# Kernel optimization log

Hardware: AMD Instinct MI355X
Metric: run time of the kernel (lower is better)

The kernel has to match this reference:

```python
import jax, jax.numpy as jnp
import numpy as np

K = 3        # prediction_steps
SKIP = 1     # skip_step (forward default)
NEG = 64     # opt.negative_samples
EPS = 1e-11  # ExpNLLLoss epsilon


def setup_inputs() -> dict:
    key = jax.random.key(0)
    ks = jax.random.split(key, 8)
    B, C, H, W = 64, 256, 14, 14
    z = jax.random.normal(ks[0], (B, C, H, W), jnp.float32)
    c = jax.random.normal(ks[1], (B, C, H, W), jnp.float32)
    Wk = jax.random.normal(ks[2], (K, C, C), jnp.float32) / np.sqrt(C).astype(np.float32)
    inp = {"z": z, "c": c, "Wk": Wk}
    for k in range(1, K + 1):
        Hp = H - (k + SKIP)
        rows = Hp * W * B
        inp[f"neg_idx_k{k}"] = jax.random.randint(ks[2 + k], (rows * NEG,), 0, rows, dtype=jnp.int32)
    return inp


def _loss_k(z, c, Wk, neg_idx, k):
    # z, c: [B,C,H,W]; Wk: [Co,Ci] (1x1 conv); neg_idx: [(H-k-SKIP)*W*B*NEG]
    B, C, H, W = z.shape
    Hp = H - (k + SKIP)
    zt = z[:, :, k + SKIP:, :]                            # [B,Ci,Hp,W]
    ztwk = jnp.einsum('oc,bchw->hwbo', Wk, zt)            # [Hp,W,B,Co] (1x1 conv + permute(2,3,0,1))
    flat = ztwk.reshape(Hp * W * B, -1)
    shuf = flat[neg_idx].reshape(Hp, W, B, NEG, -1)       # gathered negatives [Hp,W,B,N,Co]
    ctx = jnp.transpose(c[:, :, :Hp, :], (2, 3, 0, 1))    # context c[:,:,:-(k+SKIP),:] -> [Hp,W,B,Co]
    main = jnp.einsum('hwbc,hwbc->hwb', ctx, ztwk)[..., None]   # [Hp,W,B,1]
    negs = jnp.einsum('hwbc,hwbnc->hwbn', ctx, shuf)            # [Hp,W,B,N]
    log_fk = jnp.concatenate([main, negs], axis=-1)             # [Hp,W,B,1+N]
    log_fk = jnp.transpose(log_fk, (2, 3, 0, 1))                # [B,1+N,Hp,W]
    probs = jax.nn.softmax(log_fk, axis=1)
    # ExpNLLLoss, target class 0, reduction='mean'
    return -jnp.mean(jnp.log(probs[:, 0] + EPS))


def reference(z, c, Wk, neg_idx_k1, neg_idx_k2, neg_idx_k3):
    idxs = [neg_idx_k1, neg_idx_k2, neg_idx_k3]
    total = 0.0
    for k in range(1, K + 1):
        total = total + _loss_k(z, c, Wk[k - 1], idxs[k - 1], k)
    return total / K
```

## Files before the change

kernel.cpp:

```cpp
#include <hip/hip_runtime.h>
#include <math.h>


typedef short bf16x8 __attribute__((ext_vector_type(8)));
typedef float f32x4 __attribute__((ext_vector_type(4)));

static __device__ __forceinline__ unsigned short f2bf(float f) {
    union { float f; unsigned int u; } x; x.f = f;
    unsigned int r = x.u + 0x7fffu + ((x.u >> 16) & 1u);
    return (unsigned short)(r >> 16);
}

static __device__ __forceinline__ unsigned char f2e4m3(float f) {
    union { float f; unsigned int u; } x; x.f = f;
    unsigned int s = (x.u >> 24) & 0x80u;
    float af = fabsf(f);
    if (af > 448.f) af = 448.f;
    x.f = af;
    unsigned int u = x.u;
    int e = (int)(u >> 23) - 127;
    unsigned int out;
    if (af == 0.f) {
        out = 0u;
    } else if (e < -6) {
        int mq = (int)rintf(af * 512.f);
        out = (mq >= 8) ? 0x08u : (unsigned int)mq;
    } else {
        unsigned int r = u + 0x7FFFFu + ((u >> 20) & 1u);
        int e2 = (int)(r >> 23) - 127;
        if (e2 > 8) out = 0x7Eu;
        else out = (unsigned int)(((e2 + 7) << 3) | ((r >> 20) & 7u));
    }
    return (unsigned char)(s | out);
}

static __device__ __forceinline__ void gload_lds4(const void* g, void* l) {
    __builtin_amdgcn_global_load_lds(
        (const __attribute__((address_space(1))) void*)g,
        (__attribute__((address_space(3))) void*)l, 4, 0, 0);
}

__global__ __launch_bounds__(256)
void prep_kernel(const float* __restrict__ z, const float* __restrict__ c,
                 const float* __restrict__ Wk,
                 unsigned short* __restrict__ zt, unsigned char* __restrict__ ct8,
                 unsigned short* __restrict__ wkb, float* __restrict__ out) {
    __shared__ float tile[16][201];
    const int tid = threadIdx.x;
    int x = blockIdx.x;
    if (x < 768) {
        int i = x * 256 + tid;
        wkb[i] = f2bf(Wk[i]);
        if (x == 0 && tid == 0) out[0] = 0.f;
        return;
    }
    const bool isz = x < 1792;
    const int local = isz ? (x - 768) : (x - 1792);
    const float* src = isz ? z : c;
    const int b  = local & 63;
    const int c0 = (local >> 6) << 4;
    for (int i = tid; i < 16 * 196; i += 256) {
        int cc = i / 196;
        int hw = i - cc * 196;
        tile[cc][hw] = src[(size_t)((b << 8) + c0 + cc) * 196 + hw];
    }
    __syncthreads();
    if (isz) {
        for (int i = tid; i < 196 * 16; i += 256) {
            int hw = i >> 4, cc = i & 15;
            zt[(size_t)((hw << 6) + b) * 256 + c0 + cc] = f2bf(tile[cc][hw]);
        }
    } else {
        for (int i = tid; i < 196 * 16; i += 256) {
            int hw = i >> 4, cc = i & 15;
            ct8[(size_t)((hw << 6) + b) * 256 + c0 + cc] = f2e4m3(tile[cc][hw]);
        }
    }
}

#define PSTR 544
__global__ __launch_bounds__(256)
void proj_mfma_kernel(const unsigned short* __restrict__ zt,
                      const unsigned short* __restrict__ wkb,
                      unsigned char* __restrict__ ztwk) {
    __shared__ __align__(16) unsigned char smem[(64 + 32) * PSTR];
    unsigned char* smA = smem;
    unsigned char* smB = smem + 64 * PSTR;

    int x = blockIdx.x;
    int k, hw;
    if (x < 168)      { k = 0; hw = x; }
    else if (x < 322) { k = 1; hw = x - 168; }
    else              { k = 2; hw = x - 322; }
    const int o0 = blockIdx.y << 5;
    const int row0  = hw << 6;
    const int zrow0 = row0 + (((k + 2) * 14) << 6);
    unsigned char* zo = ztwk + (size_t)k * 10752 * 256;

    const int tid = threadIdx.x;
    const unsigned char* zsrc = (const unsigned char*)(zt + (size_t)zrow0 * 256);
    const unsigned char* bsrc = (const unsigned char*)(wkb + ((size_t)k << 16) + o0 * 256);

    #pragma unroll
    for (int i = 0; i < 8; ++i) {
        int sb = ((i << 8) + tid) << 4;
        int r = sb >> 9, off = sb & 511;
        *(int4*)(smA + r * PSTR + off) = *(const int4*)(zsrc + sb);
    }
    #pragma unroll
    for (int i = 0; i < 4; ++i) {
        int sb = ((i << 8) + tid) << 4;
        int r = sb >> 9, off = sb & 511;
        *(int4*)(smB + r * PSTR + off) = *(const int4*)(bsrc + sb);
    }
    __syncthreads();

    const int wv = tid >> 6, lane = tid & 63;
    const int m = lane & 15, kq = lane >> 4;
    f32x4 acc[2] = {};
    const unsigned short* aP  = (const unsigned short*)(smA + (size_t)((wv << 4) + m) * PSTR) + (kq << 3);
    const unsigned short* bP0 = (const unsigned short*)(smB + (size_t)m * PSTR) + (kq << 3);
    const unsigned short* bP1 = (const unsigned short*)(smB + (size_t)(16 + m) * PSTR) + (kq << 3);
    #pragma unroll
    for (int kk = 0; kk < 256; kk += 32) {
        bf16x8 af = *(const bf16x8*)(aP  + kk);
        bf16x8 b0 = *(const bf16x8*)(bP0 + kk);
        bf16x8 b1 = *(const bf16x8*)(bP1 + kk);
        acc[0] = __builtin_amdgcn_mfma_f32_16x16x32_bf16(af, b0, acc[0], 0, 0, 0);
        acc[1] = __builtin_amdgcn_mfma_f32_16x16x32_bf16(af, b1, acc[1], 0, 0, 0);
    }
    __syncthreads();
    unsigned char* cs = smA;
    #pragma unroll
    for (int nt = 0; nt < 2; ++nt)
        #pragma unroll
        for (int r = 0; r < 4; ++r)
            cs[(size_t)((wv << 4) + (kq << 2) + r) * 40 + (nt << 4) + m] =
                f2e4m3(acc[nt][r]);
    __syncthreads();
    {
        int r = tid >> 2, off = (tid & 3) << 3;
        unsigned long long v = *(const unsigned long long*)(cs + (size_t)r * 40 + off);
        *(unsigned long long*)(zo + (size_t)(row0 + r) * 256 + o0 + off) = v;
    }
}

#define ROWB 272
#define SLABSZ (65 * ROWB + 272)
__global__ __launch_bounds__(128)
void loss_mfma_kernel(const unsigned char* __restrict__ ct8,
                      const unsigned char* __restrict__ ztwk8,
                      const int* __restrict__ n0, const int* __restrict__ n1,
                      const int* __restrict__ n2, float* __restrict__ rowloss) {
    __shared__ __align__(16) unsigned char lds[2][SLABSZ];
    const int tid = threadIdx.x;
    const int wv = tid >> 6, lane = tid & 63;
    const int m = lane & 15, kq = lane >> 4;
    unsigned char* sl  = lds[wv];
    unsigned char* ctx = sl + 65 * ROWB;

    const int W = (blockIdx.x << 1) + wv;
    const int base = W << 3;
    int k; const int* nb; int segbase;
    if (base < 10752)      { k = 0; nb = n0; segbase = 0; }
    else if (base < 20608) { k = 1; nb = n1; segbase = 10752; }
    else                   { k = 2; nb = n2; segbase = 20608; }
    const int row0 = base - segbase;
    const unsigned char* flat8 = ztwk8 + (size_t)k * 10752 * 256;
    const float wkf = (k == 0) ? (1.f / (3.f * 10752.f))
                    : (k == 1) ? (1.f / (3.f * 9856.f))
                               : (1.f / (3.f * 8960.f));

    int soff[5];
    #pragma unroll
    for (int mt = 0; mt < 5; ++mt) {
        int slot = (mt << 4) + m;
        if (slot > 64) slot = 64;
        soff[mt] = slot * ROWB + (kq << 3);
    }

    int myidx = nb[((size_t)row0 << 6) + lane];

    for (int t = 0; t < 8; ++t) {
        const int row = row0 + t;
        asm volatile("s_waitcnt lgkmcnt(0)" ::: "memory");
        gload_lds4(flat8 + (size_t)row * 256 + (lane << 2), sl);
        gload_lds4(ct8 + (size_t)row * 256 + (lane << 2), ctx);
        #pragma unroll
        for (int j = 1; j <= 64; ++j) {
            int idx = __builtin_amdgcn_readlane(myidx, j - 1);
            gload_lds4(flat8 + (size_t)idx * 256 + (lane << 2), sl + j * ROWB);
        }
        asm volatile("s_waitcnt vmcnt(0)" ::: "memory");
        if (t + 1 < 8)
            myidx = nb[((size_t)(row + 1) << 6) + lane];

        f32x4 acc[5] = {};
        const unsigned char* cp = ctx + (kq << 3);
        #pragma unroll
        for (int kk = 0; kk < 8; ++kk) {
            long long bfrag = *(const long long*)(cp + (kk << 5));
            #pragma unroll
            for (int mt = 0; mt < 5; ++mt) {
                long long af = *(const long long*)(sl + soff[mt] + (kk << 5));
                acc[mt] = __builtin_amdgcn_mfma_f32_16x16x32_fp8_fp8(
                    af, bfrag, acc[mt], 0, 0, 0);
            }
        }

        float m_l = -1e30f;
        #pragma unroll
        for (int mt = 0; mt < 4; ++mt)
            #pragma unroll
            for (int r = 0; r < 4; ++r) m_l = fmaxf(m_l, acc[mt][r]);
        if (kq == 0) m_l = fmaxf(m_l, acc[4][0]);
        m_l = fmaxf(m_l, __shfl_xor(m_l, 16));
        m_l = fmaxf(m_l, __shfl_xor(m_l, 32));
        float s_l = 0.f;
        #pragma unroll
        for (int mt = 0; mt < 4; ++mt)
            #pragma unroll
            for (int r = 0; r < 4; ++r) s_l += __expf(acc[mt][r] - m_l);
        if (kq == 0) s_l += __expf(acc[4][0] - m_l);
        s_l += __shfl_xor(s_l, 16);
        s_l += __shfl_xor(s_l, 32);
        if (lane == 0) {
            float p0 = __expf(acc[0][0] - m_l) / s_l;
            rowloss[base + t] = -logf(p0 + 1e-11f) * wkf;
        }
    }
}

__global__ __launch_bounds__(256)
void reduce_kernel(const float* __restrict__ rl, float* __restrict__ out) {
    float s = 0.f;
    const int stride = gridDim.x * blockDim.x;
    for (int i = blockIdx.x * blockDim.x + threadIdx.x; i < 29568; i += stride)
        s += rl[i];
    #pragma unroll
    for (int off = 32; off >= 1; off >>= 1) s += __shfl_xor(s, off);
    if ((threadIdx.x & 63) == 0) atomicAdd(out, s);
}

extern "C" void kernel_launch(void* const* d_in, const int* in_sizes, int n_in,
                              void* d_out, int out_size, void* d_ws, size_t ws_size,
                              hipStream_t stream) {
    const float* z  = (const float*)d_in[0];
    const float* c  = (const float*)d_in[1];
    const float* Wk = (const float*)d_in[2];
    const int* negs[3] = {(const int*)d_in[3], (const int*)d_in[4], (const int*)d_in[5]};
    float* out = (float*)d_out;

    char* p = (char*)d_ws;
    unsigned short* zt      = (unsigned short*)p;   p += (size_t)196 * 64 * 256 * 2;
    unsigned short* wkb     = (unsigned short*)p;   p += (size_t)3 * 65536 * 2;
    unsigned char*  ct8     = (unsigned char*)p;    p += (size_t)196 * 64 * 256;
    unsigned char*  ztwk8   = (unsigned char*)p;    p += (size_t)3 * 10752 * 256;
    float*          rowloss = (float*)p;

    prep_kernel<<<2816, 256, 0, stream>>>(z, c, Wk, zt, ct8, wkb, out);
    proj_mfma_kernel<<<dim3(462, 8), 256, 0, stream>>>(zt, wkb, ztwk8);
    loss_mfma_kernel<<<1848, 128, 0, stream>>>(ct8, ztwk8, negs[0], negs[1],
                                               negs[2], rowloss);
    reduce_kernel<<<32, 256, 0, stream>>>(rowloss, out);
}
```

Before: 169.0 us.

## Software-pipeline loss kernel gathers with triple-buffered 16-row LDS groups

```diff
diff --git a/kernel.cpp b/kernel.cpp
--- a/kernel.cpp
+++ b/kernel.cpp
@@ -40,6 +40,19 @@
         (__attribute__((address_space(3))) void*)l, 4, 0, 0);
 }
 
+static __device__ __forceinline__ void wait_vmcnt_32() {
+    asm volatile("s_waitcnt vmcnt(32)" ::: "memory");
+}
+static __device__ __forceinline__ void wait_vmcnt_16() {
+    asm volatile("s_waitcnt vmcnt(16)" ::: "memory");
+}
+static __device__ __forceinline__ void wait_vmcnt_0() {
+    asm volatile("s_waitcnt vmcnt(0)" ::: "memory");
+}
+static __device__ __forceinline__ void fence_lgkm0() {
+    asm volatile("s_waitcnt lgkmcnt(0)" ::: "memory");
+}
+
 __global__ __launch_bounds__(256)
 void prep_kernel(const float* __restrict__ z, const float* __restrict__ c,
                  const float* __restrict__ Wk,
@@ -145,22 +158,19 @@
     }
 }
 
-#define ROWB 272
-#define SLABSZ (65 * ROWB + 272)
-__global__ __launch_bounds__(128)
+#define GROWB 272
+#define GBUF (16 * GROWB)
+__global__ __launch_bounds__(64)
 void loss_mfma_kernel(const unsigned char* __restrict__ ct8,
                       const unsigned char* __restrict__ ztwk8,
                       const int* __restrict__ n0, const int* __restrict__ n1,
                       const int* __restrict__ n2, float* __restrict__ rowloss) {
-    __shared__ __align__(16) unsigned char lds[2][SLABSZ];
-    const int tid = threadIdx.x;
-    const int wv = tid >> 6, lane = tid & 63;
+    __shared__ __align__(16) unsigned char buf[3][GBUF];
+    __shared__ __align__(16) unsigned char head[2][2 * GROWB];
+    const int lane = threadIdx.x;
     const int m = lane & 15, kq = lane >> 4;
-    unsigned char* sl  = lds[wv];
-    unsigned char* ctx = sl + 65 * ROWB;
-
-    const int W = (blockIdx.x << 1) + wv;
-    const int base = W << 3;
+
+    const int base = blockIdx.x << 3;
     int k; const int* nb; int segbase;
     if (base < 10752)      { k = 0; nb = n0; segbase = 0; }
     else if (base < 20608) { k = 1; nb = n1; segbase = 10752; }
@@ -171,62 +181,110 @@
                     : (k == 1) ? (1.f / (3.f * 9856.f))
                                : (1.f / (3.f * 8960.f));
 
-    int soff[5];
-    #pragma unroll
-    for (int mt = 0; mt < 5; ++mt) {
-        int slot = (mt << 4) + m;
-        if (slot > 64) slot = 64;
-        soff[mt] = slot * ROWB + (kq << 3);
-    }
-
-    int myidx = nb[((size_t)row0 << 6) + lane];
-
+    int idxv[8];
+    #pragma unroll
+    for (int t = 0; t < 8; ++t)
+        idxv[t] = nb[((size_t)(row0 + t) << 6) + lane];
+
+    const unsigned int laneoff = lane << 2;
+
+    {
+        gload_lds4(ct8 + (size_t)row0 * 256 + laneoff, &head[0][0]);
+        int g4i = __builtin_amdgcn_readlane(idxv[0], 63);
+        gload_lds4(flat8 + (size_t)g4i * 256 + laneoff, &head[0][GROWB]);
+        #pragma unroll
+        for (int r = 0; r < 16; ++r) {
+            int ridx = (r == 0) ? row0 : __builtin_amdgcn_readlane(idxv[0], r - 1);
+            gload_lds4(flat8 + (size_t)ridx * 256 + laneoff, &buf[0][r * GROWB]);
+        }
+        #pragma unroll
+        for (int r = 0; r < 16; ++r) {
+            int ridx = __builtin_amdgcn_readlane(idxv[0], 15 + r);
+            gload_lds4(flat8 + (size_t)ridx * 256 + laneoff, &buf[1][r * GROWB]);
+        }
+    }
+
+    long long ctxr[8];
+    f32x4 acc[5];
+
+    #pragma unroll
     for (int t = 0; t < 8; ++t) {
-        const int row = row0 + t;
-        asm volatile("s_waitcnt lgkmcnt(0)" ::: "memory");
-        gload_lds4(flat8 + (size_t)row * 256 + (lane << 2), sl);
-        gload_lds4(ct8 + (size_t)row * 256 + (lane << 2), ctx);
         #pragma unroll
-        for (int j = 1; j <= 64; ++j) {
-            int idx = __builtin_amdgcn_readlane(myidx, j - 1);
-            gload_lds4(flat8 + (size_t)idx * 256 + (lane << 2), sl + j * ROWB);
-        }
-        asm volatile("s_waitcnt vmcnt(0)" ::: "memory");
-        if (t + 1 < 8)
-            myidx = nb[((size_t)(row + 1) << 6) + lane];
-
-        f32x4 acc[5] = {};
-        const unsigned char* cp = ctx + (kq << 3);
-        #pragma unroll
-        for (int kk = 0; kk < 8; ++kk) {
-            long long bfrag = *(const long long*)(cp + (kk << 5));
-            #pragma unroll
-            for (int mt = 0; mt < 5; ++mt) {
-                long long af = *(const long long*)(sl + soff[mt] + (kk << 5));
-                acc[mt] = __builtin_amdgcn_mfma_f32_16x16x32_fp8_fp8(
-                    af, bfrag, acc[mt], 0, 0, 0);
+        for (int g = 0; g < 5; ++g) {
+            if (g < 4) {
+                const int q = (t << 2) + g;
+                if (q + 2 <= 31) {
+                    const int q2 = q + 2;
+                    const int t2 = q2 >> 2, g2 = q2 & 3;
+                    fence_lgkm0();
+                    if (g2 == 0) {
+                        int hrow = row0 + t2;
+                        gload_lds4(ct8 + (size_t)hrow * 256 + laneoff,
+                                   &head[t2 & 1][0]);
+                        int g4i = __builtin_amdgcn_readlane(idxv[t2], 63);
+                        gload_lds4(flat8 + (size_t)g4i * 256 + laneoff,
+                                   &head[t2 & 1][GROWB]);
+                    }
+                    const int bi2 = q2 % 3;
+                    #pragma unroll
+                    for (int r = 0; r < 16; ++r) {
+                        int slot = (g2 << 4) + r;
+                        int ridx = (slot == 0) ? (row0 + t2)
+                                 : __builtin_amdgcn_readlane(idxv[t2], slot - 1);
+                        gload_lds4(flat8 + (size_t)ridx * 256 + laneoff,
+                                   &buf[bi2][r * GROWB]);
+                    }
+                }
+                if (q <= 29)      wait_vmcnt_32();
+                else if (q == 30) wait_vmcnt_16();
+                else              wait_vmcnt_0();
+
+                if (g == 0) {
+                    #pragma unroll
+                    for (int kk = 0; kk < 8; ++kk)
+                        ctxr[kk] = *(const long long*)(
+                            &head[t & 1][(kq << 3) + (kk << 5)]);
+                    #pragma unroll
+                    for (int i = 0; i < 5; ++i)
+                        acc[i] = (f32x4){0.f, 0.f, 0.f, 0.f};
+                }
+                const int bi = q % 3;
+                #pragma unroll
+                for (int kk = 0; kk < 8; ++kk) {
+                    long long af = *(const long long*)(
+                        &buf[bi][m * GROWB + (kq << 3) + (kk << 5)]);
+                    acc[g] = __builtin_amdgcn_mfma_f32_16x16x32_fp8_fp8(
+                        af, ctxr[kk], acc[g], 0, 0, 0);
+                }
+            } else {
+                #pragma unroll
+                for (int kk = 0; kk < 8; ++kk) {
+                    long long af = *(const long long*)(
+                        &head[t & 1][GROWB + (kq << 3) + (kk << 5)]);
+                    acc[4] = __builtin_amdgcn_mfma_f32_16x16x32_fp8_fp8(
+                        af, ctxr[kk], acc[4], 0, 0, 0);
+                }
+                float m_l = -1e30f;
+                #pragma unroll
+                for (int mt = 0; mt < 4; ++mt)
+                    #pragma unroll
+                    for (int r = 0; r < 4; ++r) m_l = fmaxf(m_l, acc[mt][r]);
+                if (kq == 0) m_l = fmaxf(m_l, acc[4][0]);
+                m_l = fmaxf(m_l, __shfl_xor(m_l, 16));
+                m_l = fmaxf(m_l, __shfl_xor(m_l, 32));
+                float s_l = 0.f;
+                #pragma unroll
+                for (int mt = 0; mt < 4; ++mt)
+                    #pragma unroll
+                    for (int r = 0; r < 4; ++r) s_l += __expf(acc[mt][r] - m_l);
+                if (kq == 0) s_l += __expf(acc[4][0] - m_l);
+                s_l += __shfl_xor(s_l, 16);
+                s_l += __shfl_xor(s_l, 32);
+                if (lane == 0) {
+                    float p0 = __expf(acc[0][0] - m_l) / s_l;
+                    rowloss[base + t] = -logf(p0 + 1e-11f) * wkf;
+                }
             }
-        }
-
-        float m_l = -1e30f;
-        #pragma unroll
-        for (int mt = 0; mt < 4; ++mt)
-            #pragma unroll
-            for (int r = 0; r < 4; ++r) m_l = fmaxf(m_l, acc[mt][r]);
-        if (kq == 0) m_l = fmaxf(m_l, acc[4][0]);
-        m_l = fmaxf(m_l, __shfl_xor(m_l, 16));
-        m_l = fmaxf(m_l, __shfl_xor(m_l, 32));
-        float s_l = 0.f;
-        #pragma unroll
-        for (int mt = 0; mt < 4; ++mt)
-            #pragma unroll
-            for (int r = 0; r < 4; ++r) s_l += __expf(acc[mt][r] - m_l);
-        if (kq == 0) s_l += __expf(acc[4][0] - m_l);
-        s_l += __shfl_xor(s_l, 16);
-        s_l += __shfl_xor(s_l, 32);
-        if (lane == 0) {
-            float p0 = __expf(acc[0][0] - m_l) / s_l;
-            rowloss[base + t] = -logf(p0 + 1e-11f) * wkf;
         }
     }
 }
@@ -260,7 +318,7 @@
 
     prep_kernel<<<2816, 256, 0, stream>>>(z, c, Wk, zt, ct8, wkb, out);
     proj_mfma_kernel<<<dim3(462, 8), 256, 0, stream>>>(zt, wkb, ztwk8);
-    loss_mfma_kernel<<<1848, 128, 0, stream>>>(ct8, ztwk8, negs[0], negs[1],
-                                               negs[2], rowloss);
+    loss_mfma_kernel<<<3696, 64, 0, stream>>>(ct8, ztwk8, negs[0], negs[1],
+                                              negs[2], rowloss);
     reduce_kernel<<<32, 256, 0, stream>>>(rowloss, out);
 }
```

Result: faster. 162.8 us (-3.7%).
